# Optimization experiments

Measured on AMD Instinct MI355X. Metric: run time of the kernel, lower is better.

## Reference

```python
import jax, jax.numpy as jnp
import numpy as np

N, E, F_IN, HID, HEADS, OUT_DIM, G = 50000, 600000, 92, 32, 8, 1, 512
EPS = 1e-5


def setup_inputs() -> dict:
    key = jax.random.key(0)
    ks = jax.random.split(key, 30)
    s = 0.1
    d1 = HID * HEADS  # 256
    inp = {
        "x": jax.random.normal(ks[0], (N, F_IN), dtype=jnp.float32),
        "edge_index": jax.random.randint(ks[1], (2, E), 0, N),
        "edge_attr": jax.random.uniform(ks[2], (E, 1), dtype=jnp.float32),
        "batch": jnp.sort(jax.random.randint(ks[3], (N,), 0, G)),
        # conv1 (heads=8, concat)
        "W1": jax.random.normal(ks[4], (F_IN, d1)) * s,
        "We1": jax.random.normal(ks[5], (1, d1)) * s,
        "as1": jax.random.normal(ks[6], (HEADS, HID)) * s,
        "ad1": jax.random.normal(ks[7], (HEADS, HID)) * s,
        "ae1": jax.random.normal(ks[8], (HEADS, HID)) * s,
        "b1": jax.random.normal(ks[9], (d1,)) * s,
        # bn1 (eval mode, running stats)
        "g1": jnp.ones((d1,)), "be1": jnp.zeros((d1,)),
        "m1": jax.random.normal(ks[10], (d1,)) * s, "v1": jnp.ones((d1,)),
        # conv2 (heads=1)
        "W2": jax.random.normal(ks[11], (d1, HID)) * s,
        "We2": jax.random.normal(ks[12], (1, HID)) * s,
        "as2": jax.random.normal(ks[13], (1, HID)) * s,
        "ad2": jax.random.normal(ks[14], (1, HID)) * s,
        "ae2": jax.random.normal(ks[15], (1, HID)) * s,
        "b2": jax.random.normal(ks[16], (HID,)) * s,
        # bn2
        "g2": jnp.ones((HID,)), "be2": jnp.zeros((HID,)),
        "m2": jax.random.normal(ks[17], (HID,)) * s, "v2": jnp.ones((HID,)),
        # final fc
        "fcW": jax.random.normal(ks[18], (HID, OUT_DIM)) * s,
        "fcb": jnp.zeros((OUT_DIM,)),
    }
    return inp


def _gat_conv(x, edge_index, edge_attr, W, We, a_s, a_d, a_e, b, heads, ch):
    """PyG GATConv with edge_dim, add_self_loops=True (fill_value='mean'), concat."""
    n = x.shape[0]
    src, dst = edge_index[0], edge_index[1]
    # self loops: loop edge_attr = mean of incoming edge_attr per node
    cnt = jax.ops.segment_sum(jnp.ones((edge_attr.shape[0],), edge_attr.dtype), dst, n)
    loop_attr = jax.ops.segment_sum(edge_attr, dst, n) / jnp.clip(cnt, 1.0)[:, None]
    ar = jnp.arange(n)
    src = jnp.concatenate([src, ar])
    dst = jnp.concatenate([dst, ar])
    ea = jnp.concatenate([edge_attr, loop_attr], axis=0)
    h = (x @ W).reshape(n, heads, ch)                 # [N,H,C]
    al_s = jnp.sum(h * a_s, axis=-1)                  # [N,H]
    al_d = jnp.sum(h * a_d, axis=-1)                  # [N,H]
    he = (ea @ We).reshape(-1, heads, ch)             # [E',H,C]
    al_e = jnp.sum(he * a_e, axis=-1)                 # [E',H]
    alpha = jax.nn.leaky_relu(al_s[src] + al_d[dst] + al_e, 0.2)
    # scatter softmax over destination segments
    mx = jax.ops.segment_max(alpha, dst, n)
    w = jnp.exp(alpha - mx[dst])
    den = jax.ops.segment_sum(w, dst, n)
    w = w / den[dst]                                  # [E',H]
    out = jax.ops.segment_sum(h[src] * w[:, :, None], dst, n)  # [N,H,C]
    return out.reshape(n, heads * ch) + b


def _bn_eval(x, g, b, m, v):
    return (x - m) * (g / jnp.sqrt(v + EPS)) + b


def reference(x, edge_index, edge_attr, batch,
              W1, We1, as1, ad1, ae1, b1, g1, be1, m1, v1,
              W2, We2, as2, ad2, ae2, b2, g2, be2, m2, v2,
              fcW, fcb):
    h = _gat_conv(x, edge_index, edge_attr, W1, We1, as1, ad1, ae1, b1, HEADS, HID)
    h = jax.nn.relu(_bn_eval(h, g1, be1, m1, v1))
    # dropout is identity in eval mode
    h = _gat_conv(h, edge_index, edge_attr, W2, We2, as2, ad2, ae2, b2, 1, HID)
    h = jax.nn.relu(_bn_eval(h, g2, be2, m2, v2))
    # global mean pool over graphs
    sums = jax.ops.segment_sum(h, batch, G)
    cnt = jax.ops.segment_sum(jnp.ones((h.shape[0],), h.dtype), batch, G)
    pooled = sums / jnp.clip(cnt, 1.0)[:, None]
    return pooled @ fcW + fcb
```

## Files before the change

kernel.cpp:

```cpp
#include <hip/hip_runtime.h>
#include <hip/hip_bf16.h>

#define N_NODES 50000
#define N_EDGES 600000
#define F_IN    92
#define KPAD    96
#define HID     32
#define HEADS   8
#define D1      256
#define G_GRAPHS 512
#define EPSV    1e-5f
#define NCHUNK  49
#define DEGBLK  2344

using short8  = __attribute__((ext_vector_type(8))) short;
using f32x4   = __attribute__((ext_vector_type(4))) float;
using f32x2   = __attribute__((ext_vector_type(2))) float;

__device__ __forceinline__ float bf2f(unsigned short u) {
    return __uint_as_float(((unsigned)u) << 16);
}
__device__ __forceinline__ unsigned short f2bf(float f) {
    unsigned u = __float_as_uint(f);
    return (unsigned short)((u + 0x7FFFu + ((u >> 16) & 1u)) >> 16);
}


__global__ __launch_bounds__(256) void k_deg_setup(
        const int* __restrict__ ei, int* __restrict__ deg,
        const float* __restrict__ W1, const float* __restrict__ W2,
        const float* __restrict__ We1, const float* __restrict__ ae1,
        const float* __restrict__ We2, const float* __restrict__ ae2,
        const float* __restrict__ as1, const float* __restrict__ ad1,
        const float* __restrict__ b1, const float* __restrict__ g1,
        const float* __restrict__ be1, const float* __restrict__ m1,
        const float* __restrict__ v1,
        const float* __restrict__ b2, const float* __restrict__ g2,
        const float* __restrict__ be2, const float* __restrict__ m2,
        const float* __restrict__ v2,
        unsigned short* __restrict__ W1p, unsigned short* __restrict__ W2p,
        float* __restrict__ va, float* __restrict__ wedot,
        float* __restrict__ bnA1, float* __restrict__ bnB1,
        float* __restrict__ bnA2, float* __restrict__ bnB2) {
    int blk = blockIdx.x, t = threadIdx.x;
    if (blk < DEGBLK) {
        int e = blk * 256 + t;
        if (e < N_EDGES) atomicAdd(&deg[ei[N_EDGES + e]], 1);
        return;
    }
    int b = blk - DEGBLK;
    if (b < 96) {
        int gid = b * 256 + t;
        int k = gid >> 8, col = gid & 255;
        unsigned short v = 0;
        if (k < F_IN) v = f2bf(W1[k * D1 + col]);
        W1p[(((k >> 3) * D1) + col) * 8 + (k & 7)] = v;
    } else if (b < 128) {
        int gid = (b - 96) * 256 + t;
        int k = gid >> 5, col = gid & 31;
        W2p[(((k >> 3) * 32) + col) * 8 + (k & 7)] = f2bf(W2[gid]);
    } else if (b < 134) {
        int gid = (b - 128) * 256 + t;
        if (gid < 2 * HEADS * F_IN) {
            int which = gid / (HEADS * F_IN), rem = gid % (HEADS * F_IN);
            int h = rem / F_IN, k = rem % F_IN;
            const float* av = which ? ad1 : as1;
            float s = 0.f;
            #pragma unroll 8
            for (int c = 0; c < HID; ++c) s += W1[k * D1 + h * HID + c] * av[h * HID + c];
            va[gid] = s;
        }
    } else if (b == 134) {
        if (t < HEADS) {
            float a = 0.f;
            for (int c = 0; c < HID; ++c) a += We1[t * HID + c] * ae1[t * HID + c];
            wedot[t] = a;
        } else if (t == HEADS) {
            float a = 0.f;
            for (int c = 0; c < HID; ++c) a += We2[c] * ae2[c];
            wedot[HEADS] = a;
        }
    } else {
        if (t < D1) {
            float sc = g1[t] * __frsqrt_rn(v1[t] + EPSV);
            bnA1[t] = sc;
            bnB1[t] = (b1[t] - m1[t]) * sc + be1[t];
        }
        if (t < HID) {
            float sc = g2[t] * __frsqrt_rn(v2[t] + EPSV);
            bnA2[t] = sc;
            bnB2[t] = (b2[t] - m2[t]) * sc + be2[t];
        }
    }
}

__global__ void k_partial(const int* __restrict__ deg, int* __restrict__ partials) {
    int b = blockIdx.x;
    int s = 0;
    for (int j = 0; j < 4; ++j) {
        int i = b * 1024 + j * 256 + threadIdx.x;
        if (i < N_NODES) s += deg[i];
    }
    for (int off = 32; off; off >>= 1) s += __shfl_down(s, off, 64);
    __shared__ int sm[4];
    if ((threadIdx.x & 63) == 0) sm[threadIdx.x >> 6] = s;
    __syncthreads();
    if (threadIdx.x == 0) partials[b] = sm[0] + sm[1] + sm[2] + sm[3];
}

__global__ void k_scanc(const int* __restrict__ deg, const int* __restrict__ partials,
                        int* __restrict__ row_off, int* __restrict__ cursor) {
    int b = blockIdx.x;
    int t = threadIdx.x;
    __shared__ int smp;
    if (t < 64) {
        int pv = (t < b) ? partials[t] : 0;
        #pragma unroll
        for (int off = 32; off; off >>= 1) pv += __shfl_down(pv, off, 64);
        if (t == 0) smp = pv;
    }
    int base_i = b * 1024 + t * 4;
    int v[4]; int s = 0;
    #pragma unroll
    for (int j = 0; j < 4; ++j) {
        int i = base_i + j;
        v[j] = (i < N_NODES) ? deg[i] : 0;
        s += v[j];
    }
    __shared__ int sm[256];
    sm[t] = s;
    __syncthreads();
    int val = s;
    for (int off = 1; off < 256; off <<= 1) {
        int add = (t >= off) ? sm[t - off] : 0;
        __syncthreads();
        val += add;
        sm[t] = val;
        __syncthreads();
    }
    int base = smp + (val - s);
    #pragma unroll
    for (int j = 0; j < 4; ++j) {
        int i = base_i + j;
        if (i < N_NODES) { row_off[i] = base; cursor[i] = base; }
        base += v[j];
    }
}

__global__ void k_fill(const int* __restrict__ ei, const float* __restrict__ ea,
                       int* __restrict__ cursor, int2* __restrict__ adj) {
    int e = blockIdx.x * 256 + threadIdx.x;
    if (e < N_EDGES) {
        int d = ei[N_EDGES + e];
        int pos = atomicAdd(&cursor[d], 1);
        adj[pos] = make_int2(ei[e], __float_as_int(ea[e]));
    }
}

__global__ __launch_bounds__(256) void k_conv1(const float* __restrict__ x,
                                               const unsigned short* __restrict__ W1p,
                                               const float* __restrict__ va,
                                               unsigned char* __restrict__ h1f8,
                                               float* __restrict__ al_s,
                                               float* __restrict__ al_d) {
    __shared__ float xs[16 * F_IN];
    __shared__ unsigned short xbs[16 * KPAD];
    __shared__ float hs[16 * D1];
    int n0 = blockIdx.x * 16;
    int t = threadIdx.x;
    for (int i = t; i < 16 * F_IN; i += 256)
        xs[i] = x[(size_t)n0 * F_IN + i];
    __syncthreads();
    for (int i = t; i < 16 * KPAD; i += 256) {
        int r = i / KPAD, k = i - r * KPAD;
        xbs[i] = (k < F_IN) ? f2bf(xs[r * F_IN + k]) : (unsigned short)0;
    }
    {
        int r = t >> 4, j = t & 15;
        const float* vp = va + j * F_IN;
        const float* xr = xs + r * F_IN;
        float s = 0.f;
        for (int k = 0; k < F_IN; ++k) s += xr[k] * vp[k];
        if (j < 8) al_s[(n0 + r) * HEADS + j] = s;
        else       al_d[(n0 + r) * HEADS + (j - 8)] = s;
    }
    __syncthreads();
    int wid = t >> 6, l = t & 63;
    int g = l >> 4, c16 = l & 15;
    const short8* xb = (const short8*)(xbs + c16 * KPAD + g * 8);
    short8 af0 = xb[0], af1 = xb[4], af2 = xb[8];
    const short8* wp = (const short8*)W1p;
    #pragma unroll
    for (int ct = 0; ct < 4; ++ct) {
        int col = (wid * 4 + ct) * 16 + c16;
        f32x4 acc = {0.f, 0.f, 0.f, 0.f};
        acc = __builtin_amdgcn_mfma_f32_16x16x32_bf16(af0, wp[(0 * 4 + g) * D1 + col], acc, 0, 0, 0);
        acc = __builtin_amdgcn_mfma_f32_16x16x32_bf16(af1, wp[(1 * 4 + g) * D1 + col], acc, 0, 0, 0);
        acc = __builtin_amdgcn_mfma_f32_16x16x32_bf16(af2, wp[(2 * 4 + g) * D1 + col], acc, 0, 0, 0);
        #pragma unroll
        for (int r = 0; r < 4; ++r)
            hs[(g * 4 + r) * D1 + col] = acc[r];
    }
    __syncthreads();
    {
        int r = t >> 4, grp = t & 15;
        const float* src = hs + r * D1 + grp * 16;
        int d[4];
        #pragma unroll
        for (int j = 0; j < 4; ++j) {
            int lo = __builtin_amdgcn_cvt_pk_fp8_f32(src[j * 4 + 0], src[j * 4 + 1], 0, false);
            d[j]   = __builtin_amdgcn_cvt_pk_fp8_f32(src[j * 4 + 2], src[j * 4 + 3], lo, true);
        }
        *(int4*)(h1f8 + (size_t)(n0 + r) * D1 + grp * 16) = make_int4(d[0], d[1], d[2], d[3]);
    }
}

__global__ __launch_bounds__(256) void k_aggr1(
        const int* __restrict__ row_off, const int* __restrict__ deg,
        const int2* __restrict__ adj,
        const unsigned char* __restrict__ h1f8,
        const float* __restrict__ al_s, const float* __restrict__ al_d,
        const float* __restrict__ wedot,
        const float* __restrict__ bnA1, const float* __restrict__ bnB1,
        unsigned short* __restrict__ h1p) {
    int wid = threadIdx.x >> 6, l = threadIdx.x & 63;
    int n = blockIdx.x * 4 + wid;
    if (n >= N_NODES) return;
    int h = l >> 3;
    float wd = wedot[h];
    float dn = al_d[n * HEADS + h];
    int r0 = row_off[n], cnt = deg[n];
    float a0 = 0.f, a1 = 0.f, a2 = 0.f, a3 = 0.f, den = 0.f, ea_sum = 0.f;
    for (int base = 0; base < cnt; base += 64) {
        int m = cnt - base; if (m > 64) m = 64;
        int sl = 0; float el = 0.f;
        if (l < m) {
            int2 se = adj[r0 + base + l];
            sl = se.x;
            el = __int_as_float(se.y);
        }
        for (int i = 0; i < m; ++i) {
            int s = __shfl(sl, i, 64);
            float eav = __shfl(el, i, 64);
            float a = al_s[s * HEADS + h] + dn + eav * wd;
            a = a > 0.f ? a : 0.2f * a;
            float w = __expf(a);
            den += w;
            ea_sum += eav;
            unsigned w8 = *(const unsigned*)(h1f8 + (size_t)s * D1 + l * 4);
            f32x2 lo = __builtin_amdgcn_cvt_pk_f32_fp8(w8, false);
            f32x2 hi = __builtin_amdgcn_cvt_pk_f32_fp8(w8, true);
            a0 += w * lo.x; a1 += w * lo.y;
            a2 += w * hi.x; a3 += w * hi.y;
        }
    }
    {
        float la = ea_sum / (float)(cnt > 0 ? cnt : 1);
        float a = al_s[n * HEADS + h] + dn + la * wd;
        a = a > 0.f ? a : 0.2f * a;
        float w = __expf(a);
        den += w;
        unsigned w8 = *(const unsigned*)(h1f8 + (size_t)n * D1 + l * 4);
        f32x2 lo = __builtin_amdgcn_cvt_pk_f32_fp8(w8, false);
        f32x2 hi = __builtin_amdgcn_cvt_pk_f32_fp8(w8, true);
        a0 += w * lo.x; a1 += w * lo.y;
        a2 += w * hi.x; a3 += w * hi.y;
    }
    float inv = 1.f / den;
    int c = l * 4;
    float4 A = *(const float4*)(bnA1 + c);
    float4 B = *(const float4*)(bnB1 + c);
    ushort4 o;
    o.x = f2bf(fmaxf(a0 * inv * A.x + B.x, 0.f));
    o.y = f2bf(fmaxf(a1 * inv * A.y + B.y, 0.f));
    o.z = f2bf(fmaxf(a2 * inv * A.z + B.z, 0.f));
    o.w = f2bf(fmaxf(a3 * inv * A.w + B.w, 0.f));
    *(ushort4*)(h1p + (size_t)n * D1 + c) = o;
}


__global__ __launch_bounds__(256) void k_gemm2(const unsigned short* __restrict__ h1p,
                                               const unsigned short* __restrict__ W2p,
                                               const float* __restrict__ as2,
                                               const float* __restrict__ ad2,
                                               unsigned short* __restrict__ h2b,
                                               float* __restrict__ al_s2,
                                               float* __restrict__ al_d2) {
    int wid = threadIdx.x >> 6, l = threadIdx.x & 63;
    int wave = blockIdx.x * 4 + wid;
    if (wave >= N_NODES / 16) return;
    int n0 = wave * 16;
    int g = l >> 4;
    int c16 = l & 15;
    f32x4 acc0 = {0.f, 0.f, 0.f, 0.f};
    f32x4 acc1 = {0.f, 0.f, 0.f, 0.f};
    const short8* ap = (const short8*)(h1p + (size_t)(n0 + c16) * D1 + g * 8);
    const short8* wp = (const short8*)W2p;
    #pragma unroll
    for (int ks = 0; ks < 8; ++ks) {
        short8 afrag = ap[ks * 4];
        short8 b0 = wp[(ks * 4 + g) * 32 + c16];
        short8 b1 = wp[(ks * 4 + g) * 32 + 16 + c16];
        acc0 = __builtin_amdgcn_mfma_f32_16x16x32_bf16(afrag, b0, acc0, 0, 0, 0);
        acc1 = __builtin_amdgcn_mfma_f32_16x16x32_bf16(afrag, b1, acc1, 0, 0, 0);
    }
    float s0 = as2[c16], s1 = as2[16 + c16];
    float d0 = ad2[c16], d1 = ad2[16 + c16];
    float ps[4], pd[4];
    #pragma unroll
    for (int r = 0; r < 4; ++r) {
        int node = n0 + g * 4 + r;
        h2b[(size_t)node * HID + c16]      = f2bf(acc0[r]);
        h2b[(size_t)node * HID + 16 + c16] = f2bf(acc1[r]);
        ps[r] = acc0[r] * s0 + acc1[r] * s1;
        pd[r] = acc0[r] * d0 + acc1[r] * d1;
    }
    #pragma unroll
    for (int off = 1; off < 16; off <<= 1) {
        #pragma unroll
        for (int r = 0; r < 4; ++r) {
            ps[r] += __shfl_xor(ps[r], off, 64);
            pd[r] += __shfl_xor(pd[r], off, 64);
        }
    }
    if (c16 == 0) {
        #pragma unroll
        for (int r = 0; r < 4; ++r) {
            int node = n0 + g * 4 + r;
            al_s2[node] = ps[r];
            al_d2[node] = pd[r];
        }
    }
}

__global__ __launch_bounds__(256) void k_aggr2(
        const int* __restrict__ row_off, const int* __restrict__ deg,
        const int2* __restrict__ adj,
        const unsigned short* __restrict__ h2b,
        const float* __restrict__ al_s2, const float* __restrict__ al_d2,
        const float* __restrict__ wedot,
        const float* __restrict__ bnA2, const float* __restrict__ bnB2,
        float* __restrict__ h2p) {
    int wid = threadIdx.x >> 6, l = threadIdx.x & 63;
    int n = blockIdx.x * 4 + wid;
    if (n >= N_NODES) return;
    int q = l >> 4, c2 = l & 15;
    float wd = wedot[HEADS];
    float dn = al_d2[n];
    int r0 = row_off[n], cnt = deg[n];
    float acc0 = 0.f, acc1 = 0.f, den = 0.f, ea_sum = 0.f;
    for (int base = 0; base < cnt; base += 64) {
        int m = cnt - base; if (m > 64) m = 64;
        int sl = 0; float el = 0.f;
        if (l < m) {
            int2 se = adj[r0 + base + l];
            sl = se.x;
            el = __int_as_float(se.y);
        }
        for (int i = 0; i < m; i += 4) {
            int j = i + q;
            int jj = j < m ? j : 0;
            int s = __shfl(sl, jj, 64);
            float eav = __shfl(el, jj, 64);
            if (j < m) {
                float a = al_s2[s] + dn + eav * wd;
                a = a > 0.f ? a : 0.2f * a;
                float w = __expf(a);
                den += w;
                ea_sum += eav;
                ushort2 p = *(const ushort2*)(h2b + (size_t)s * HID + c2 * 2);
                acc0 += w * bf2f(p.x);
                acc1 += w * bf2f(p.y);
            }
        }
    }
    acc0 += __shfl_xor(acc0, 16, 64); acc0 += __shfl_xor(acc0, 32, 64);
    acc1 += __shfl_xor(acc1, 16, 64); acc1 += __shfl_xor(acc1, 32, 64);
    den  += __shfl_xor(den, 16, 64);  den  += __shfl_xor(den, 32, 64);
    ea_sum += __shfl_xor(ea_sum, 16, 64); ea_sum += __shfl_xor(ea_sum, 32, 64);
    {
        float la = ea_sum / (float)(cnt > 0 ? cnt : 1);
        float a = al_s2[n] + dn + la * wd;
        a = a > 0.f ? a : 0.2f * a;
        float w = __expf(a);
        den += w;
        ushort2 p = *(const ushort2*)(h2b + (size_t)n * HID + c2 * 2);
        acc0 += w * bf2f(p.x);
        acc1 += w * bf2f(p.y);
    }
    int c = c2 * 2;
    float inv = 1.f / den;
    float y0 = fmaxf(acc0 * inv * bnA2[c] + bnB2[c], 0.f);
    float y1 = fmaxf(acc1 * inv * bnA2[c + 1] + bnB2[c + 1], 0.f);
    if (q == 0) {
        float2 st = {y0, y1};
        *(float2*)(h2p + (size_t)n * HID + c) = st;
    }
}

__global__ __launch_bounds__(64) void k_poolfc(const float* __restrict__ h2p,
                                               const int* __restrict__ batch,
                                               const float* __restrict__ fcW,
                                               const float* __restrict__ fcb,
                                               float* __restrict__ out) {
    int g = blockIdx.x;
    int l = threadIdx.x;
    auto lb = [&](int key) {
        int lo = 0, hi = N_NODES;
        while (lo < hi) {
            int mid = (lo + hi) >> 1;
            if (batch[mid] < key) lo = mid + 1; else hi = mid;
        }
        return lo;
    };
    int s0 = lb(g), s1 = lb(g + 1);
    int c = l & 31, half = l >> 5;
    float acc = 0.f;
    for (int r = s0 + half; r < s1; r += 2)
        acc += h2p[(size_t)r * HID + c];
    acc += __shfl_xor(acc, 32, 64);
    int cn = s1 - s0;
    float mean = acc / (float)(cn > 0 ? cn : 1);
    float p = mean * fcW[c];
    #pragma unroll
    for (int off = 1; off < 32; off <<= 1) p += __shfl_xor(p, off, 64);
    if (l == 0) out[g] = p + fcb[0];
}


extern "C" void kernel_launch(void* const* d_in, const int* in_sizes, int n_in,
                              void* d_out, int out_size, void* d_ws, size_t ws_size,
                              hipStream_t stream) {
    const float* x    = (const float*)d_in[0];
    const int*   ei   = (const int*)  d_in[1];
    const float* ea   = (const float*)d_in[2];
    const int*   batch= (const int*)  d_in[3];
    const float* W1   = (const float*)d_in[4];
    const float* We1  = (const float*)d_in[5];
    const float* as1  = (const float*)d_in[6];
    const float* ad1  = (const float*)d_in[7];
    const float* ae1  = (const float*)d_in[8];
    const float* b1   = (const float*)d_in[9];
    const float* g1   = (const float*)d_in[10];
    const float* be1  = (const float*)d_in[11];
    const float* m1   = (const float*)d_in[12];
    const float* v1   = (const float*)d_in[13];
    const float* W2   = (const float*)d_in[14];
    const float* We2  = (const float*)d_in[15];
    const float* as2  = (const float*)d_in[16];
    const float* ad2  = (const float*)d_in[17];
    const float* ae2  = (const float*)d_in[18];
    const float* b2   = (const float*)d_in[19];
    const float* g2   = (const float*)d_in[20];
    const float* be2  = (const float*)d_in[21];
    const float* m2   = (const float*)d_in[22];
    const float* v2   = (const float*)d_in[23];
    const float* fcW  = (const float*)d_in[24];
    const float* fcb  = (const float*)d_in[25];
    float* out = (float*)d_out;

    char* ws = (char*)d_ws;
    size_t off = 0;
    auto alloc = [&](size_t bytes) -> void* {
        void* p = ws + off;
        off += (bytes + 255) & ~(size_t)255;
        return p;
    };
    int*   deg     = (int*)  alloc((size_t)N_NODES * 4);
    int*   row_off = (int*)  alloc((size_t)N_NODES * 4);
    int*   cursor  = (int*)  alloc((size_t)N_NODES * 4);
    int2*  adj     = (int2*) alloc((size_t)N_EDGES * 8);
    float* al_s1   = (float*)alloc((size_t)N_NODES * HEADS * 4);
    float* al_d1   = (float*)alloc((size_t)N_NODES * HEADS * 4);
    float* al_s2   = (float*)alloc((size_t)N_NODES * 4);
    float* al_d2   = (float*)alloc((size_t)N_NODES * 4);
    float* wedot   = (float*)alloc(16 * 4);
    float* va      = (float*)alloc((size_t)2 * HEADS * F_IN * 4);
    int*   partials= (int*)  alloc(64 * 4);
    float* bnA1    = (float*)alloc((size_t)D1 * 4);
    float* bnB1    = (float*)alloc((size_t)D1 * 4);
    float* bnA2    = (float*)alloc((size_t)HID * 4);
    float* bnB2    = (float*)alloc((size_t)HID * 4);
    unsigned short* W1p = (unsigned short*)alloc((size_t)KPAD * D1 * 2);
    unsigned short* W2p = (unsigned short*)alloc((size_t)D1 * HID * 2);
    unsigned char*  h1f8 = (unsigned char*)alloc((size_t)N_NODES * D1);
    unsigned short* h1p = (unsigned short*)alloc((size_t)N_NODES * D1 * 2);
    unsigned short* h2b = (unsigned short*)alloc((size_t)N_NODES * HID * 2);
    float* h2p     = (float*)alloc((size_t)N_NODES * HID * 4);
    (void)ws_size; (void)in_sizes; (void)n_in; (void)out_size;

    hipMemsetAsync(deg, 0, (size_t)N_NODES * 4, stream);

    k_deg_setup<<<DEGBLK + 136, 256, 0, stream>>>(ei, deg, W1, W2, We1, ae1, We2, ae2,
                                                  as1, ad1, b1, g1, be1, m1, v1,
                                                  b2, g2, be2, m2, v2,
                                                  W1p, W2p, va, wedot,
                                                  bnA1, bnB1, bnA2, bnB2);
    k_partial<<<NCHUNK, 256, 0, stream>>>(deg, partials);
    k_scanc<<<NCHUNK, 256, 0, stream>>>(deg, partials, row_off, cursor);
    k_fill<<<(N_EDGES + 255) / 256, 256, 0, stream>>>(ei, ea, cursor, adj);

    k_conv1<<<N_NODES / 16, 256, 0, stream>>>(x, W1p, va, h1f8, al_s1, al_d1);
    k_aggr1<<<(N_NODES + 3) / 4, 256, 0, stream>>>(row_off, deg, adj,
                                                   h1f8, al_s1, al_d1, wedot,
                                                   bnA1, bnB1, h1p);

    k_gemm2<<<(N_NODES / 16 + 3) / 4, 256, 0, stream>>>(h1p, W2p, as2, ad2, h2b, al_s2, al_d2);
    k_aggr2<<<(N_NODES + 3) / 4, 256, 0, stream>>>(row_off, deg, adj,
                                                   h2b, al_s2, al_d2, wedot, bnA2, bnB2, h2p);
    k_poolfc<<<G_GRAPHS, 64, 0, stream>>>(h2p, batch, fcW, fcb, out);
}
```

Before: 218.2 us.

## Store conv2 features as FP8 and fuse edge fill with conv1 launch

Conv2 features are now stored as FP8 instead of bf16, which halves the gather traffic in the second aggregation. That kernel is reshaped so each lane handles four channels and eight edges are processed in parallel per wave. Separately, the CSR fill and the conv1 GEMM are merged into one launch using a block-index split, which removes one launch and lets the two run concurrently. The cost is lower precision for the conv2 features and a larger shared-memory footprint on the fill blocks, which may reduce their occupancy.

```diff
diff --git a/kernel.cpp b/kernel.cpp
--- a/kernel.cpp
+++ b/kernel.cpp
@@ -12,6 +12,7 @@
 #define EPSV    1e-5f
 #define NCHUNK  49
 #define DEGBLK  2344
+#define FILLBLK 2344
 
 using short8  = __attribute__((ext_vector_type(8))) short;
 using f32x4   = __attribute__((ext_vector_type(4))) float;
@@ -147,27 +148,29 @@
     }
 }
 
-__global__ void k_fill(const int* __restrict__ ei, const float* __restrict__ ea,
-                       int* __restrict__ cursor, int2* __restrict__ adj) {
-    int e = blockIdx.x * 256 + threadIdx.x;
-    if (e < N_EDGES) {
-        int d = ei[N_EDGES + e];
-        int pos = atomicAdd(&cursor[d], 1);
-        adj[pos] = make_int2(ei[e], __float_as_int(ea[e]));
-    }
-}
-
-__global__ __launch_bounds__(256) void k_conv1(const float* __restrict__ x,
-                                               const unsigned short* __restrict__ W1p,
-                                               const float* __restrict__ va,
-                                               unsigned char* __restrict__ h1f8,
-                                               float* __restrict__ al_s,
-                                               float* __restrict__ al_d) {
+__global__ __launch_bounds__(256) void k_fill_conv1(
+        const int* __restrict__ ei, const float* __restrict__ ea,
+        int* __restrict__ cursor, int2* __restrict__ adj,
+        const float* __restrict__ x,
+        const unsigned short* __restrict__ W1p,
+        const float* __restrict__ va,
+        unsigned char* __restrict__ h1f8,
+        float* __restrict__ al_s,
+        float* __restrict__ al_d) {
     __shared__ float xs[16 * F_IN];
     __shared__ unsigned short xbs[16 * KPAD];
     __shared__ float hs[16 * D1];
-    int n0 = blockIdx.x * 16;
     int t = threadIdx.x;
+    if (blockIdx.x < FILLBLK) {
+        int e = blockIdx.x * 256 + t;
+        if (e < N_EDGES) {
+            int d = ei[N_EDGES + e];
+            int pos = atomicAdd(&cursor[d], 1);
+            adj[pos] = make_int2(ei[e], __float_as_int(ea[e]));
+        }
+        return;
+    }
+    int n0 = (blockIdx.x - FILLBLK) * 16;
     for (int i = t; i < 16 * F_IN; i += 256)
         xs[i] = x[(size_t)n0 * F_IN + i];
     __syncthreads();
@@ -283,7 +286,7 @@
                                                const unsigned short* __restrict__ W2p,
                                                const float* __restrict__ as2,
                                                const float* __restrict__ ad2,
-                                               unsigned short* __restrict__ h2b,
+                                               unsigned char* __restrict__ h2f8,
                                                float* __restrict__ al_s2,
                                                float* __restrict__ al_d2) {
     int wid = threadIdx.x >> 6, l = threadIdx.x & 63;
@@ -310,8 +313,10 @@
     #pragma unroll
     for (int r = 0; r < 4; ++r) {
         int node = n0 + g * 4 + r;
-        h2b[(size_t)node * HID + c16]      = f2bf(acc0[r]);
-        h2b[(size_t)node * HID + 16 + c16] = f2bf(acc1[r]);
+        int p0 = __builtin_amdgcn_cvt_pk_fp8_f32(acc0[r], acc0[r], 0, false);
+        int p1 = __builtin_amdgcn_cvt_pk_fp8_f32(acc1[r], acc1[r], 0, false);
+        h2f8[(size_t)node * HID + c16]      = (unsigned char)p0;
+        h2f8[(size_t)node * HID + 16 + c16] = (unsigned char)p1;
         ps[r] = acc0[r] * s0 + acc1[r] * s1;
         pd[r] = acc0[r] * d0 + acc1[r] * d1;
     }
@@ -336,7 +341,7 @@
 __global__ __launch_bounds__(256) void k_aggr2(
         const int* __restrict__ row_off, const int* __restrict__ deg,
         const int2* __restrict__ adj,
-        const unsigned short* __restrict__ h2b,
+        const unsigned char* __restrict__ h2f8,
         const float* __restrict__ al_s2, const float* __restrict__ al_d2,
         const float* __restrict__ wedot,
         const float* __restrict__ bnA2, const float* __restrict__ bnB2,
@@ -344,11 +349,11 @@
     int wid = threadIdx.x >> 6, l = threadIdx.x & 63;
     int n = blockIdx.x * 4 + wid;
     if (n >= N_NODES) return;
-    int q = l >> 4, c2 = l & 15;
+    int g = l >> 3, c8 = l & 7;
     float wd = wedot[HEADS];
     float dn = al_d2[n];
     int r0 = row_off[n], cnt = deg[n];
-    float acc0 = 0.f, acc1 = 0.f, den = 0.f, ea_sum = 0.f;
+    float a0 = 0.f, a1 = 0.f, a2 = 0.f, a3 = 0.f, den = 0.f, ea_sum = 0.f;
     for (int base = 0; base < cnt; base += 64) {
         int m = cnt - base; if (m > 64) m = 64;
         int sl = 0; float el = 0.f;
@@ -357,8 +362,8 @@
             sl = se.x;
             el = __int_as_float(se.y);
         }
-        for (int i = 0; i < m; i += 4) {
-            int j = i + q;
+        for (int i = 0; i < m; i += 8) {
+            int j = i + g;
             int jj = j < m ? j : 0;
             int s = __shfl(sl, jj, 64);
             float eav = __shfl(el, jj, 64);
@@ -368,33 +373,46 @@
                 float w = __expf(a);
                 den += w;
                 ea_sum += eav;
-                ushort2 p = *(const ushort2*)(h2b + (size_t)s * HID + c2 * 2);
-                acc0 += w * bf2f(p.x);
-                acc1 += w * bf2f(p.y);
+                unsigned w8 = *(const unsigned*)(h2f8 + (size_t)s * HID + c8 * 4);
+                f32x2 lo = __builtin_amdgcn_cvt_pk_f32_fp8(w8, false);
+                f32x2 hi = __builtin_amdgcn_cvt_pk_f32_fp8(w8, true);
+                a0 += w * lo.x; a1 += w * lo.y;
+                a2 += w * hi.x; a3 += w * hi.y;
             }
         }
     }
-    acc0 += __shfl_xor(acc0, 16, 64); acc0 += __shfl_xor(acc0, 32, 64);
-    acc1 += __shfl_xor(acc1, 16, 64); acc1 += __shfl_xor(acc1, 32, 64);
-    den  += __shfl_xor(den, 16, 64);  den  += __shfl_xor(den, 32, 64);
-    ea_sum += __shfl_xor(ea_sum, 16, 64); ea_sum += __shfl_xor(ea_sum, 32, 64);
+    #pragma unroll
+    for (int off = 8; off < 64; off <<= 1) {
+        a0 += __shfl_xor(a0, off, 64);
+        a1 += __shfl_xor(a1, off, 64);
+        a2 += __shfl_xor(a2, off, 64);
+        a3 += __shfl_xor(a3, off, 64);
+        den += __shfl_xor(den, off, 64);
+        ea_sum += __shfl_xor(ea_sum, off, 64);
+    }
     {
         float la = ea_sum / (float)(cnt > 0 ? cnt : 1);
         float a = al_s2[n] + dn + la * wd;
         a = a > 0.f ? a : 0.2f * a;
         float w = __expf(a);
         den += w;
-        ushort2 p = *(const ushort2*)(h2b + (size_t)n * HID + c2 * 2);
-        acc0 += w * bf2f(p.x);
-        acc1 += w * bf2f(p.y);
-    }
-    int c = c2 * 2;
-    float inv = 1.f / den;
-    float y0 = fmaxf(acc0 * inv * bnA2[c] + bnB2[c], 0.f);
-    float y1 = fmaxf(acc1 * inv * bnA2[c + 1] + bnB2[c + 1], 0.f);
-    if (q == 0) {
-        float2 st = {y0, y1};
-        *(float2*)(h2p + (size_t)n * HID + c) = st;
+        unsigned w8 = *(const unsigned*)(h2f8 + (size_t)n * HID + c8 * 4);
+        f32x2 lo = __builtin_amdgcn_cvt_pk_f32_fp8(w8, false);
+        f32x2 hi = __builtin_amdgcn_cvt_pk_f32_fp8(w8, true);
+        a0 += w * lo.x; a1 += w * lo.y;
+        a2 += w * hi.x; a3 += w * hi.y;
+    }
+    if (g == 0) {
+        float inv = 1.f / den;
+        int c = c8 * 4;
+        float4 A = *(const float4*)(bnA2 + c);
+        float4 B = *(const float4*)(bnB2 + c);
+        float4 y;
+        y.x = fmaxf(a0 * inv * A.x + B.x, 0.f);
+        y.y = fmaxf(a1 * inv * A.y + B.y, 0.f);
+        y.z = fmaxf(a2 * inv * A.z + B.z, 0.f);
+        y.w = fmaxf(a3 * inv * A.w + B.w, 0.f);
+        *(float4*)(h2p + (size_t)n * HID + c) = y;
     }
 }
 
@@ -485,7 +503,7 @@
     unsigned short* W2p = (unsigned short*)alloc((size_t)D1 * HID * 2);
     unsigned char*  h1f8 = (unsigned char*)alloc((size_t)N_NODES * D1);
     unsigned short* h1p = (unsigned short*)alloc((size_t)N_NODES * D1 * 2);
-    unsigned short* h2b = (unsigned short*)alloc((size_t)N_NODES * HID * 2);
+    unsigned char*  h2f8 = (unsigned char*)alloc((size_t)N_NODES * HID);
     float* h2p     = (float*)alloc((size_t)N_NODES * HID * 4);
     (void)ws_size; (void)in_sizes; (void)n_in; (void)out_size;
 
@@ -498,15 +516,15 @@
                                                   bnA1, bnB1, bnA2, bnB2);
     k_partial<<<NCHUNK, 256, 0, stream>>>(deg, partials);
     k_scanc<<<NCHUNK, 256, 0, stream>>>(deg, partials, row_off, cursor);
-    k_fill<<<(N_EDGES + 255) / 256, 256, 0, stream>>>(ei, ea, cursor, adj);
-
-    k_conv1<<<N_NODES / 16, 256, 0, stream>>>(x, W1p, va, h1f8, al_s1, al_d1);
+    k_fill_conv1<<<FILLBLK + N_NODES / 16, 256, 0, stream>>>(ei, ea, cursor, adj,
+                                                             x, W1p, va, h1f8,
+                                                             al_s1, al_d1);
     k_aggr1<<<(N_NODES + 3) / 4, 256, 0, stream>>>(row_off, deg, adj,
                                                    h1f8, al_s1, al_d1, wedot,
                                                    bnA1, bnB1, h1p);
 
-    k_gemm2<<<(N_NODES / 16 + 3) / 4, 256, 0, stream>>>(h1p, W2p, as2, ad2, h2b, al_s2, al_d2);
+    k_gemm2<<<(N_NODES / 16 + 3) / 4, 256, 0, stream>>>(h1p, W2p, as2, ad2, h2f8, al_s2, al_d2);
     k_aggr2<<<(N_NODES + 3) / 4, 256, 0, stream>>>(row_off, deg, adj,
-                                                   h2b, al_s2, al_d2, wedot, bnA2, bnB2, h2p);
+                                                   h2f8, al_s2, al_d2, wedot, bnA2, bnB2, h2p);
     k_poolfc<<<G_GRAPHS, 64, 0, stream>>>(h2p, batch, fcW, fcb, out);
 }
```

New measurement: 214.1 us. About the same (-1.9%).
